# Kernel tuning notes

Measured on AMD Instinct MI355X. Metric: run time of the kernel, lower is better.

The kernel has to match this reference:

```python
import jax, jax.numpy as jnp
import numpy as np

# binarize = sign() in forward; standard BNN binarize uses a straight-through
# estimator (gradient clipped to |x|<=1) in backward. Forward math: sign.

def binarize(x):
    return jnp.sign(x)


def setup_inputs() -> dict:
    key = jax.random.key(0)
    k1, k2 = jax.random.split(key)
    M, K, N = 8192, 4096, 4096
    x = jax.random.normal(k1, (M, K), dtype=jnp.float32)
    # xavier-scale init for weight; scale is irrelevant after sign() but kept realistic
    w = jax.random.normal(k2, (K, N), dtype=jnp.float32) * np.sqrt(2.0 / (K + N)).astype(np.float32)
    return {"x": x, "weight": w}


def reference(x, weight):
    # sign-binarize activations and weights, then dense matmul
    xb = binarize(x)            # [M, K] in {-1, 0, +1}
    wb = binarize(weight)       # [K, N]
    return jnp.matmul(xb, wb)   # [M, N]
```

## Files before the change

### kernel.cpp

```cpp
#include <hip/hip_runtime.h>
#include <stdint.h>

#define M_DIM 8192
#define K_DIM 4096
#define N_DIM 4096

using i32x4 = __attribute__((ext_vector_type(4))) int;
using i32x8 = __attribute__((ext_vector_type(8))) int;
using f32x16 = __attribute__((ext_vector_type(16))) float;

typedef const __attribute__((address_space(1))) void g_void;
typedef __attribute__((address_space(3))) void lds_void;

__device__ __forceinline__ void gload_lds16(const void* g, void* l) {
  __builtin_amdgcn_global_load_lds((g_void*)g, (lds_void*)l, 16, 0, 0);
}

__device__ __forceinline__ void barrier_raw() {
  asm volatile("" ::: "memory");
  __builtin_amdgcn_s_barrier();
  asm volatile("" ::: "memory");
}

__device__ __forceinline__ unsigned code4(float v) {
  return v > 0.f ? 0x2u : (v < 0.f ? 0xAu : 0x0u);
}

__global__ void pack_x4_kernel(const float* __restrict__ in,
                               uint8_t* __restrict__ out) {
  __shared__ __align__(16) uint16_t cds[32 * 264];
  int g = blockIdx.x;
  int tq = blockIdx.y;
  int tid = threadIdx.x;
#pragma unroll
  for (int i = 0; i < 32; ++i) {
    int flat = tid + 256 * i;
    int row = flat >> 8;
    int c4 = flat & 255;
    const float4 v = *reinterpret_cast<const float4*>(
        in + (long)(g * 32 + row) * K_DIM + tq * 1024 + c4 * 4);
    unsigned u = code4(v.x) | (code4(v.y) << 4) | (code4(v.z) << 8) |
                 (code4(v.w) << 12);
    cds[row * 264 + c4] = (uint16_t)u;
  }
  __syncthreads();
#pragma unroll
  for (int j = 0; j < 4; ++j) {
    int u = tid + 256 * j;
    int tl = u >> 7;
    int kc = (u >> 5) & 3;
    int row = u & 31;
    i32x4 val = *reinterpret_cast<const i32x4*>(&cds[row * 264 + tl * 32 + kc * 8]);
    int t = tq * 8 + tl;
    long o = ((((long)g * 32 + t) * 4 + kc) * 32 + row) * 16;
    *reinterpret_cast<i32x4*>(out + o) = val;
  }
}

__global__ void pack_wt4_kernel(const float* __restrict__ w,
                                uint8_t* __restrict__ out) {
  __shared__ __align__(16) uint8_t tile[64 * 144];
  int n0 = blockIdx.x * 64;
  int k0 = blockIdx.y * 128;
  int tid = threadIdx.x;
#pragma unroll
  for (int i = 0; i < 32; ++i) {
    int flat = tid + 256 * i;
    int r = flat >> 6;
    int c = flat & 63;
    tile[c * 144 + r] = (uint8_t)code4(w[(long)(k0 + r) * N_DIM + n0 + c]);
  }
  __syncthreads();
  int rg = tid >> 7, kc = (tid >> 5) & 3, row = tid & 31;
  const unsigned* sp =
      reinterpret_cast<const unsigned*>(&tile[(rg * 32 + row) * 144 + kc * 32]);
  i32x4 val;
#pragma unroll
  for (int d = 0; d < 4; ++d) {
    unsigned s0 = sp[2 * d], s1 = sp[2 * d + 1];
    unsigned t0 = s0 & 0x0F0F0F0Fu, t1 = s1 & 0x0F0F0F0Fu;
    unsigned p = (t0 | (t0 >> 4)) & 0x00FF00FFu;
    unsigned q = (t1 | (t1 >> 4)) & 0x00FF00FFu;
    val[d] = (int)((p & 0xFFu) | ((p >> 8) & 0xFF00u) | ((q & 0xFFu) << 16) |
                   ((q >> 16) << 24));
  }
  int g = (n0 >> 5) + rg;
  int t = k0 >> 7;
  long o = ((((long)g * 32 + t) * 4 + kc) * 32 + row) * 16;
  *reinterpret_cast<i32x4*>(out + o) = val;
}

__device__ __forceinline__ i32x8 lo8(i32x4 r) {
  return __builtin_shufflevector(r, r, 0, 1, 2, 3, -1, -1, -1, -1);
}

#define SCALE1 0x7f7f7f7f

template <int VM, bool ISSUE, int CUR>
__device__ __forceinline__ void tile_step(
    int t, const uint8_t* __restrict__ gA, const uint8_t* __restrict__ gB0,
    const uint8_t* __restrict__ gB1, int dstA, int dstB, uint8_t* lds,
    int aRd, int bRd, f32x16 (&acc)[4][2]) {
  const uint8_t* buf = lds + CUR * 24576;
  constexpr int SN = (CUR + 2) % 3;
  if (ISSUE) {
    long kn = (long)(t + 2) * 2048;
    uint8_t* nbuf = lds + SN * 24576;
    gload_lds16(gA + kn, nbuf + dstA);
    gload_lds16(gA + kn + 1024, nbuf + dstA + 1024);
    gload_lds16(gB0 + kn, nbuf + dstB);
    gload_lds16(gB0 + kn + 1024, nbuf + dstB + 1024);
    gload_lds16(gB1 + kn, nbuf + dstB + 2048);
    gload_lds16(gB1 + kn + 1024, nbuf + dstB + 3072);
  }
  i32x4 a0[4], b0[2], a1[4], b1[2];
#pragma unroll
  for (int mi = 0; mi < 4; ++mi)
    a0[mi] = *reinterpret_cast<const i32x4*>(buf + aRd + mi * 2048);
#pragma unroll
  for (int ni = 0; ni < 2; ++ni)
    b0[ni] = *reinterpret_cast<const i32x4*>(buf + bRd + ni * 2048);
#pragma unroll
  for (int mi = 0; mi < 4; ++mi)
    a1[mi] = *reinterpret_cast<const i32x4*>(buf + aRd + mi * 2048 + 1024);
#pragma unroll
  for (int ni = 0; ni < 2; ++ni)
    b1[ni] = *reinterpret_cast<const i32x4*>(buf + bRd + ni * 2048 + 1024);
  asm volatile("s_waitcnt lgkmcnt(6)" ::: "memory");
  __builtin_amdgcn_sched_barrier(0);
  __builtin_amdgcn_s_setprio(1);
#pragma unroll
  for (int mi = 0; mi < 4; ++mi)
#pragma unroll
    for (int ni = 0; ni < 2; ++ni)
      acc[mi][ni] = __builtin_amdgcn_mfma_scale_f32_32x32x64_f8f6f4(
          lo8(a0[mi]), lo8(b0[ni]), acc[mi][ni], 4, 4, 0, SCALE1, 0, SCALE1);
  __builtin_amdgcn_s_setprio(0);
  asm volatile("s_waitcnt lgkmcnt(0)" ::: "memory");
  __builtin_amdgcn_sched_barrier(0);
  __builtin_amdgcn_s_setprio(1);
#pragma unroll
  for (int mi = 0; mi < 4; ++mi)
#pragma unroll
    for (int ni = 0; ni < 2; ++ni)
      acc[mi][ni] = __builtin_amdgcn_mfma_scale_f32_32x32x64_f8f6f4(
          lo8(a1[mi]), lo8(b1[ni]), acc[mi][ni], 4, 4, 0, SCALE1, 0, SCALE1);
  __builtin_amdgcn_s_setprio(0);
  if (VM >= 0) {
    if (VM == 6) asm volatile("s_waitcnt vmcnt(6)" ::: "memory");
    else asm volatile("s_waitcnt vmcnt(0)" ::: "memory");
    barrier_raw();
  }
}

__global__ __launch_bounds__(256, 2) void gemm_fp4_kernel(
    const uint8_t* __restrict__ A, const uint8_t* __restrict__ B,
    float* __restrict__ C) {
  __shared__ __align__(16) uint8_t lds[3 * 24576];

  int bid = blockIdx.x;
  int xcd = bid & 7;
  int i = bid >> 3;
  int bn = (i & 7) + ((xcd & 1) << 3);
  int bm = (i >> 3) + ((xcd >> 1) << 4);

  int tid = threadIdx.x;
  int wid = tid >> 6;
  int lane = tid & 63;

  const uint8_t* gA = A + (long)(bm * 4 + wid) * 65536 + lane * 16;
  const uint8_t* gB0 = B + (long)(bn * 8 + 2 * wid) * 65536 + lane * 16;
  const uint8_t* gB1 = gB0 + 65536;
  int dstA = wid * 2048;
  int dstB = 8192 + wid * 4096;

  int aRd = lane * 16;
  int bRd = 8192 + (wid * 2) * 2048 + lane * 16;

  f32x16 acc[4][2] = {};

#pragma unroll
  for (int t = 0; t < 2; ++t) {
    uint8_t* buf = lds + t * 24576;
    long k0 = (long)t * 2048;
    gload_lds16(gA + k0, buf + dstA);
    gload_lds16(gA + k0 + 1024, buf + dstA + 1024);
    gload_lds16(gB0 + k0, buf + dstB);
    gload_lds16(gB0 + k0 + 1024, buf + dstB + 1024);
    gload_lds16(gB1 + k0, buf + dstB + 2048);
    gload_lds16(gB1 + k0 + 1024, buf + dstB + 3072);
  }
  asm volatile("s_waitcnt vmcnt(6)" ::: "memory");
  barrier_raw();

#pragma unroll 1
  for (int tt = 0; tt < 30; tt += 3) {
    tile_step<6, true, 0>(tt, gA, gB0, gB1, dstA, dstB, lds, aRd, bRd, acc);
    tile_step<6, true, 1>(tt + 1, gA, gB0, gB1, dstA, dstB, lds, aRd, bRd, acc);
    tile_step<6, true, 2>(tt + 2, gA, gB0, gB1, dstA, dstB, lds, aRd, bRd, acc);
  }
  tile_step<0, false, 0>(30, gA, gB0, gB1, dstA, dstB, lds, aRd, bRd, acc);
  tile_step<-1, false, 1>(31, gA, gB0, gB1, dstA, dstB, lds, aRd, bRd, acc);

  long row0 = (long)bm * 128 + ((lane >> 5) << 2);
  long col0 = (long)bn * 256 + wid * 64 + (lane & 31);
#pragma unroll
  for (int mi = 0; mi < 4; ++mi)
#pragma unroll
    for (int ni = 0; ni < 2; ++ni)
#pragma unroll
      for (int r = 0; r < 16; ++r) {
        long row = row0 + mi * 32 + (r & 3) + ((r >> 2) << 3);
        C[row * N_DIM + col0 + ni * 32] = acc[mi][ni][r];
      }
}

extern "C" void kernel_launch(void* const* d_in, const int* in_sizes, int n_in,
                              void* d_out, int out_size, void* d_ws, size_t ws_size,
                              hipStream_t stream) {
  const float* x = (const float*)d_in[0];
  const float* w = (const float*)d_in[1];
  float* out = (float*)d_out;

  uint8_t* x4 = (uint8_t*)d_ws;
  uint8_t* w4t = x4 + (size_t)M_DIM * (K_DIM / 2);

  pack_x4_kernel<<<dim3(M_DIM / 32, 4), 256, 0, stream>>>(x, x4);
  pack_wt4_kernel<<<dim3(N_DIM / 64, K_DIM / 128), 256, 0, stream>>>(w, w4t);
  gemm_fp4_kernel<<<1024, 256, 0, stream>>>(x4, w4t, out);
}
```

Before: 124.4 us.

## Prefetch next tile's LDS fragments into registers during current MFMAs

Restructures the GEMM main loop to double-buffer register fragments: while the current tile's MFMAs run, the next tile's A/B fragments are read from LDS into a second register set. The global-load wait is moved before the barrier and tightened to vmcnt(0), and the loop is unrolled by six to rotate both LDS and register buffers. This aims to hide LDS read latency behind matrix ops. In exchange it raises register pressure and waits fully on outstanding global loads each step.

```diff
diff --git a/kernel.cpp b/kernel.cpp
--- a/kernel.cpp
+++ b/kernel.cpp
@@ -96,16 +96,29 @@
 
 #define SCALE1 0x7f7f7f7f
 
-template <int VM, bool ISSUE, int CUR>
+template <int VM, bool ISSUE, bool READ, int CUR>
 __device__ __forceinline__ void tile_step(
     int t, const uint8_t* __restrict__ gA, const uint8_t* __restrict__ gB0,
     const uint8_t* __restrict__ gB1, int dstA, int dstB, uint8_t* lds,
-    int aRd, int bRd, f32x16 (&acc)[4][2]) {
-  const uint8_t* buf = lds + CUR * 24576;
-  constexpr int SN = (CUR + 2) % 3;
+    int aRd, int bRd, i32x4 (&aC)[8], i32x4 (&bC)[4], i32x4 (&aN)[8],
+    i32x4 (&bN)[4], f32x16 (&acc)[4][2]) {
+  asm volatile("s_waitcnt lgkmcnt(6)" ::: "memory");
+  __builtin_amdgcn_sched_barrier(0);
+  __builtin_amdgcn_s_setprio(1);
+#pragma unroll
+  for (int mi = 0; mi < 4; ++mi)
+#pragma unroll
+    for (int ni = 0; ni < 2; ++ni)
+      acc[mi][ni] = __builtin_amdgcn_mfma_scale_f32_32x32x64_f8f6f4(
+          lo8(aC[mi]), lo8(bC[ni]), acc[mi][ni], 4, 4, 0, SCALE1, 0, SCALE1);
+  __builtin_amdgcn_s_setprio(0);
+  if (VM >= 0) {
+    asm volatile("s_waitcnt vmcnt(0)" ::: "memory");
+    barrier_raw();
+  }
   if (ISSUE) {
     long kn = (long)(t + 2) * 2048;
-    uint8_t* nbuf = lds + SN * 24576;
+    uint8_t* nbuf = lds + ((CUR + 2) % 3) * 24576;
     gload_lds16(gA + kn, nbuf + dstA);
     gload_lds16(gA + kn + 1024, nbuf + dstA + 1024);
     gload_lds16(gB0 + kn, nbuf + dstB);
@@ -113,20 +126,25 @@
     gload_lds16(gB1 + kn, nbuf + dstB + 2048);
     gload_lds16(gB1 + kn + 1024, nbuf + dstB + 3072);
   }
-  i32x4 a0[4], b0[2], a1[4], b1[2];
-#pragma unroll
-  for (int mi = 0; mi < 4; ++mi)
-    a0[mi] = *reinterpret_cast<const i32x4*>(buf + aRd + mi * 2048);
-#pragma unroll
-  for (int ni = 0; ni < 2; ++ni)
-    b0[ni] = *reinterpret_cast<const i32x4*>(buf + bRd + ni * 2048);
-#pragma unroll
-  for (int mi = 0; mi < 4; ++mi)
-    a1[mi] = *reinterpret_cast<const i32x4*>(buf + aRd + mi * 2048 + 1024);
-#pragma unroll
-  for (int ni = 0; ni < 2; ++ni)
-    b1[ni] = *reinterpret_cast<const i32x4*>(buf + bRd + ni * 2048 + 1024);
-  asm volatile("s_waitcnt lgkmcnt(6)" ::: "memory");
+  if (READ) {
+    const uint8_t* nb = lds + ((CUR + 1) % 3) * 24576;
+#pragma unroll
+    for (int mi = 0; mi < 4; ++mi)
+      aN[mi] = *reinterpret_cast<const i32x4*>(nb + aRd + mi * 2048);
+#pragma unroll
+    for (int ni = 0; ni < 2; ++ni)
+      bN[ni] = *reinterpret_cast<const i32x4*>(nb + bRd + ni * 2048);
+#pragma unroll
+    for (int mi = 0; mi < 4; ++mi)
+      aN[4 + mi] = *reinterpret_cast<const i32x4*>(nb + aRd + mi * 2048 + 1024);
+#pragma unroll
+    for (int ni = 0; ni < 2; ++ni)
+      bN[2 + ni] = *reinterpret_cast<const i32x4*>(nb + bRd + ni * 2048 + 1024);
+  }
+  if (READ)
+    asm volatile("s_waitcnt lgkmcnt(12)" ::: "memory");
+  else
+    asm volatile("s_waitcnt lgkmcnt(0)" ::: "memory");
   __builtin_amdgcn_sched_barrier(0);
   __builtin_amdgcn_s_setprio(1);
 #pragma unroll
@@ -134,23 +152,9 @@
 #pragma unroll
     for (int ni = 0; ni < 2; ++ni)
       acc[mi][ni] = __builtin_amdgcn_mfma_scale_f32_32x32x64_f8f6f4(
-          lo8(a0[mi]), lo8(b0[ni]), acc[mi][ni], 4, 4, 0, SCALE1, 0, SCALE1);
+          lo8(aC[4 + mi]), lo8(bC[2 + ni]), acc[mi][ni], 4, 4, 0, SCALE1, 0,
+          SCALE1);
   __builtin_amdgcn_s_setprio(0);
-  asm volatile("s_waitcnt lgkmcnt(0)" ::: "memory");
-  __builtin_amdgcn_sched_barrier(0);
-  __builtin_amdgcn_s_setprio(1);
-#pragma unroll
-  for (int mi = 0; mi < 4; ++mi)
-#pragma unroll
-    for (int ni = 0; ni < 2; ++ni)
-      acc[mi][ni] = __builtin_amdgcn_mfma_scale_f32_32x32x64_f8f6f4(
-          lo8(a1[mi]), lo8(b1[ni]), acc[mi][ni], 4, 4, 0, SCALE1, 0, SCALE1);
-  __builtin_amdgcn_s_setprio(0);
-  if (VM >= 0) {
-    if (VM == 6) asm volatile("s_waitcnt vmcnt(6)" ::: "memory");
-    else asm volatile("s_waitcnt vmcnt(0)" ::: "memory");
-    barrier_raw();
-  }
 }
 
 __global__ __launch_bounds__(256, 2) void gemm_fp4_kernel(
@@ -177,6 +181,7 @@
   int aRd = lane * 16;
   int bRd = 8192 + (wid * 2) * 2048 + lane * 16;
 
+  i32x4 aA[8], bA[4], aB[8], bB[4];
   f32x16 acc[4][2] = {};
 
 #pragma unroll
@@ -192,15 +197,38 @@
   }
   asm volatile("s_waitcnt vmcnt(6)" ::: "memory");
   barrier_raw();
+#pragma unroll
+  for (int mi = 0; mi < 4; ++mi)
+    aA[mi] = *reinterpret_cast<const i32x4*>(lds + aRd + mi * 2048);
+#pragma unroll
+  for (int ni = 0; ni < 2; ++ni)
+    bA[ni] = *reinterpret_cast<const i32x4*>(lds + bRd + ni * 2048);
+#pragma unroll
+  for (int mi = 0; mi < 4; ++mi)
+    aA[4 + mi] = *reinterpret_cast<const i32x4*>(lds + aRd + mi * 2048 + 1024);
+#pragma unroll
+  for (int ni = 0; ni < 2; ++ni)
+    bA[2 + ni] = *reinterpret_cast<const i32x4*>(lds + bRd + ni * 2048 + 1024);
 
 #pragma unroll 1
-  for (int tt = 0; tt < 30; tt += 3) {
-    tile_step<6, true, 0>(tt, gA, gB0, gB1, dstA, dstB, lds, aRd, bRd, acc);
-    tile_step<6, true, 1>(tt + 1, gA, gB0, gB1, dstA, dstB, lds, aRd, bRd, acc);
-    tile_step<6, true, 2>(tt + 2, gA, gB0, gB1, dstA, dstB, lds, aRd, bRd, acc);
-  }
-  tile_step<0, false, 0>(30, gA, gB0, gB1, dstA, dstB, lds, aRd, bRd, acc);
-  tile_step<-1, false, 1>(31, gA, gB0, gB1, dstA, dstB, lds, aRd, bRd, acc);
+  for (int tt = 0; tt < 30; tt += 6) {
+    tile_step<0, true, true, 0>(tt, gA, gB0, gB1, dstA, dstB, lds, aRd, bRd,
+                                aA, bA, aB, bB, acc);
+    tile_step<0, true, true, 1>(tt + 1, gA, gB0, gB1, dstA, dstB, lds, aRd,
+                                bRd, aB, bB, aA, bA, acc);
+    tile_step<0, true, true, 2>(tt + 2, gA, gB0, gB1, dstA, dstB, lds, aRd,
+                                bRd, aA, bA, aB, bB, acc);
+    tile_step<0, true, true, 0>(tt + 3, gA, gB0, gB1, dstA, dstB, lds, aRd,
+                                bRd, aB, bB, aA, bA, acc);
+    tile_step<0, true, true, 1>(tt + 4, gA, gB0, gB1, dstA, dstB, lds, aRd,
+                                bRd, aA, bA, aB, bB, acc);
+    tile_step<0, true, true, 2>(tt + 5, gA, gB0, gB1, dstA, dstB, lds, aRd,
+                                bRd, aB, bB, aA, bA, acc);
+  }
+  tile_step<0, false, true, 0>(30, gA, gB0, gB1, dstA, dstB, lds, aRd, bRd,
+                               aA, bA, aB, bB, acc);
+  tile_step<-1, false, false, 1>(31, gA, gB0, gB1, dstA, dstB, lds, aRd, bRd,
+                                 aB, bB, aA, bA, acc);
 
   long row0 = (long)bm * 128 + ((lane >> 5) << 2);
   long col0 = (long)bn * 256 + wid * 64 + (lane & 31);
```

Result: slower. 127.0 us (+2.1%).

## Load B operand directly into registers instead of staging through LDS

Applied to the files above, without the earlier changes.

Each wave used B data only for itself, so B tiles are now fetched straight from global memory into a triple-buffered register set, and only A is staged through LDS. LDS drops from 72KB to 24KB per block and the per-step LDS reads for B go away, which could allow higher occupancy and cuts LDS traffic. In exchange there are more live VGPRs for the register buffers, and the vmcnt(6) wait is left unchanged even though the number of outstanding loads per step has changed, which may over- or under-wait.

```diff
diff --git a/kernel.cpp b/kernel.cpp
--- a/kernel.cpp
+++ b/kernel.cpp
@@ -98,35 +98,28 @@
 
 template <int VM, bool ISSUE, int CUR>
 __device__ __forceinline__ void tile_step(
-    int t, const uint8_t* __restrict__ gA, const uint8_t* __restrict__ gB0,
-    const uint8_t* __restrict__ gB1, int dstA, int dstB, uint8_t* lds,
-    int aRd, int bRd, f32x16 (&acc)[4][2]) {
-  const uint8_t* buf = lds + CUR * 24576;
-  constexpr int SN = (CUR + 2) % 3;
+    int t, const uint8_t* __restrict__ gA, const uint8_t* __restrict__ gB,
+    int dstA, uint8_t* lds, int aRd, i32x4 (&bC)[4], i32x4 (&bN)[4],
+    f32x16 (&acc)[4][2]) {
+  const uint8_t* buf = lds + CUR * 8192;
   if (ISSUE) {
     long kn = (long)(t + 2) * 2048;
-    uint8_t* nbuf = lds + SN * 24576;
+    bN[0] = *reinterpret_cast<const i32x4*>(gB + kn);
+    bN[1] = *reinterpret_cast<const i32x4*>(gB + 65536 + kn);
+    bN[2] = *reinterpret_cast<const i32x4*>(gB + kn + 1024);
+    bN[3] = *reinterpret_cast<const i32x4*>(gB + 65536 + kn + 1024);
+    uint8_t* nbuf = lds + ((CUR + 2) % 3) * 8192;
     gload_lds16(gA + kn, nbuf + dstA);
     gload_lds16(gA + kn + 1024, nbuf + dstA + 1024);
-    gload_lds16(gB0 + kn, nbuf + dstB);
-    gload_lds16(gB0 + kn + 1024, nbuf + dstB + 1024);
-    gload_lds16(gB1 + kn, nbuf + dstB + 2048);
-    gload_lds16(gB1 + kn + 1024, nbuf + dstB + 3072);
-  }
-  i32x4 a0[4], b0[2], a1[4], b1[2];
+  }
+  i32x4 a0[4], a1[4];
 #pragma unroll
   for (int mi = 0; mi < 4; ++mi)
     a0[mi] = *reinterpret_cast<const i32x4*>(buf + aRd + mi * 2048);
 #pragma unroll
-  for (int ni = 0; ni < 2; ++ni)
-    b0[ni] = *reinterpret_cast<const i32x4*>(buf + bRd + ni * 2048);
-#pragma unroll
   for (int mi = 0; mi < 4; ++mi)
     a1[mi] = *reinterpret_cast<const i32x4*>(buf + aRd + mi * 2048 + 1024);
-#pragma unroll
-  for (int ni = 0; ni < 2; ++ni)
-    b1[ni] = *reinterpret_cast<const i32x4*>(buf + bRd + ni * 2048 + 1024);
-  asm volatile("s_waitcnt lgkmcnt(6)" ::: "memory");
+  asm volatile("s_waitcnt lgkmcnt(4)" ::: "memory");
   __builtin_amdgcn_sched_barrier(0);
   __builtin_amdgcn_s_setprio(1);
 #pragma unroll
@@ -134,7 +127,7 @@
 #pragma unroll
     for (int ni = 0; ni < 2; ++ni)
       acc[mi][ni] = __builtin_amdgcn_mfma_scale_f32_32x32x64_f8f6f4(
-          lo8(a0[mi]), lo8(b0[ni]), acc[mi][ni], 4, 4, 0, SCALE1, 0, SCALE1);
+          lo8(a0[mi]), lo8(bC[ni]), acc[mi][ni], 4, 4, 0, SCALE1, 0, SCALE1);
   __builtin_amdgcn_s_setprio(0);
   asm volatile("s_waitcnt lgkmcnt(0)" ::: "memory");
   __builtin_amdgcn_sched_barrier(0);
@@ -144,7 +137,8 @@
 #pragma unroll
     for (int ni = 0; ni < 2; ++ni)
       acc[mi][ni] = __builtin_amdgcn_mfma_scale_f32_32x32x64_f8f6f4(
-          lo8(a1[mi]), lo8(b1[ni]), acc[mi][ni], 4, 4, 0, SCALE1, 0, SCALE1);
+          lo8(a1[mi]), lo8(bC[2 + ni]), acc[mi][ni], 4, 4, 0, SCALE1, 0,
+          SCALE1);
   __builtin_amdgcn_s_setprio(0);
   if (VM >= 0) {
     if (VM == 6) asm volatile("s_waitcnt vmcnt(6)" ::: "memory");
@@ -156,7 +150,7 @@
 __global__ __launch_bounds__(256, 2) void gemm_fp4_kernel(
     const uint8_t* __restrict__ A, const uint8_t* __restrict__ B,
     float* __restrict__ C) {
-  __shared__ __align__(16) uint8_t lds[3 * 24576];
+  __shared__ __align__(16) uint8_t lds[3 * 8192];
 
   int bid = blockIdx.x;
   int xcd = bid & 7;
@@ -169,38 +163,37 @@
   int lane = tid & 63;
 
   const uint8_t* gA = A + (long)(bm * 4 + wid) * 65536 + lane * 16;
-  const uint8_t* gB0 = B + (long)(bn * 8 + 2 * wid) * 65536 + lane * 16;
-  const uint8_t* gB1 = gB0 + 65536;
+  const uint8_t* gB = B + (long)(bn * 8 + 2 * wid) * 65536 + lane * 16;
   int dstA = wid * 2048;
-  int dstB = 8192 + wid * 4096;
 
   int aRd = lane * 16;
-  int bRd = 8192 + (wid * 2) * 2048 + lane * 16;
-
+
+  i32x4 bs0[4], bs1[4], bs2[4];
   f32x16 acc[4][2] = {};
 
-#pragma unroll
-  for (int t = 0; t < 2; ++t) {
-    uint8_t* buf = lds + t * 24576;
-    long k0 = (long)t * 2048;
-    gload_lds16(gA + k0, buf + dstA);
-    gload_lds16(gA + k0 + 1024, buf + dstA + 1024);
-    gload_lds16(gB0 + k0, buf + dstB);
-    gload_lds16(gB0 + k0 + 1024, buf + dstB + 1024);
-    gload_lds16(gB1 + k0, buf + dstB + 2048);
-    gload_lds16(gB1 + k0 + 1024, buf + dstB + 3072);
-  }
+  bs0[0] = *reinterpret_cast<const i32x4*>(gB);
+  bs0[1] = *reinterpret_cast<const i32x4*>(gB + 65536);
+  bs0[2] = *reinterpret_cast<const i32x4*>(gB + 1024);
+  bs0[3] = *reinterpret_cast<const i32x4*>(gB + 65536 + 1024);
+  gload_lds16(gA, lds + dstA);
+  gload_lds16(gA + 1024, lds + dstA + 1024);
+  bs1[0] = *reinterpret_cast<const i32x4*>(gB + 2048);
+  bs1[1] = *reinterpret_cast<const i32x4*>(gB + 65536 + 2048);
+  bs1[2] = *reinterpret_cast<const i32x4*>(gB + 3072);
+  bs1[3] = *reinterpret_cast<const i32x4*>(gB + 65536 + 3072);
+  gload_lds16(gA + 2048, lds + 8192 + dstA);
+  gload_lds16(gA + 3072, lds + 8192 + dstA + 1024);
   asm volatile("s_waitcnt vmcnt(6)" ::: "memory");
   barrier_raw();
 
 #pragma unroll 1
   for (int tt = 0; tt < 30; tt += 3) {
-    tile_step<6, true, 0>(tt, gA, gB0, gB1, dstA, dstB, lds, aRd, bRd, acc);
-    tile_step<6, true, 1>(tt + 1, gA, gB0, gB1, dstA, dstB, lds, aRd, bRd, acc);
-    tile_step<6, true, 2>(tt + 2, gA, gB0, gB1, dstA, dstB, lds, aRd, bRd, acc);
-  }
-  tile_step<0, false, 0>(30, gA, gB0, gB1, dstA, dstB, lds, aRd, bRd, acc);
-  tile_step<-1, false, 1>(31, gA, gB0, gB1, dstA, dstB, lds, aRd, bRd, acc);
+    tile_step<6, true, 0>(tt, gA, gB, dstA, lds, aRd, bs0, bs2, acc);
+    tile_step<6, true, 1>(tt + 1, gA, gB, dstA, lds, aRd, bs1, bs0, acc);
+    tile_step<6, true, 2>(tt + 2, gA, gB, dstA, lds, aRd, bs2, bs1, acc);
+  }
+  tile_step<0, false, 0>(30, gA, gB, dstA, lds, aRd, bs0, bs2, acc);
+  tile_step<-1, false, 1>(31, gA, gB, dstA, lds, aRd, bs1, bs0, acc);
 
   long row0 = (long)bm * 128 + ((lane >> 5) << 2);
   long col0 = (long)bn * 256 + wid * 64 + (lane & 31);
```

Result: no change. 125.4 us (+0.8%).
